# Kernel optimization log

Hardware: AMD Instinct MI355X
Metric: run time of the kernel (lower is better)

Reference implementation:

```python
import jax, jax.numpy as jnp
import numpy as np

B, L, H, E, K = 64, 200, 256, 8, 2
LN_EPS = 1e-5

def setup_inputs() -> dict:
    key = jax.random.key(0)
    ks = jax.random.split(key, 24)
    r = lambda k, *s: jax.random.normal(k, s, dtype=jnp.float32)
    w = lambda k, *s: 0.02 * jax.random.normal(k, s, dtype=jnp.float32)
    return {
        'text_emb': r(ks[0], B, L, H),
        'img_emb': r(ks[1], B, L, H),
        'item_emb': r(ks[2], B, L, H),
        'noise_t': r(ks[3], B, L, H),
        'noise_i': r(ks[4], B, L, H),
        'W_mu_t': w(ks[5], H, H), 'b_mu_t': jnp.zeros((H,), jnp.float32),
        'W_sg_t': w(ks[6], H, H), 'b_sg_t': jnp.zeros((H,), jnp.float32),
        'W_mu_i': w(ks[7], H, H), 'b_mu_i': jnp.zeros((H,), jnp.float32),
        'W_sg_i': w(ks[8], H, H), 'b_sg_i': jnp.zeros((H,), jnp.float32),
        'W_gate': w(ks[9], H, E), 'b_gate': jnp.zeros((E,), jnp.float32),
        'W_texp': w(ks[10], E, H, H), 'b_texp': jnp.zeros((E, H), jnp.float32),
        'W_iexp': w(ks[11], E, H, H), 'b_iexp': jnp.zeros((E, H), jnp.float32),
        'W_fuse': w(ks[12], 2 * H, H), 'b_fuse': jnp.zeros((H,), jnp.float32),
        'ln_g': jnp.ones((H,), jnp.float32), 'ln_b': jnp.zeros((H,), jnp.float32),
    }

def _topk_routing(z, W_gate, b_gate):
    # softmax over experts, keep top-k, renormalize (matches torch scatter_ version)
    weights = jax.nn.softmax(z @ W_gate + b_gate, axis=-1)   # [B,L,E]
    top_w, idx = jax.lax.top_k(weights, K)                   # [B,L,K]
    sparse = jnp.sum(jax.nn.one_hot(idx, E, dtype=weights.dtype) * top_w[..., None], axis=-2)
    return sparse / (jnp.sum(sparse, axis=-1, keepdims=True) + 1e-8)

def _layernorm(x, g, b):
    mu = jnp.mean(x, axis=-1, keepdims=True)
    var = jnp.mean(jnp.square(x - mu), axis=-1, keepdims=True)
    return (x - mu) * jax.lax.rsqrt(var + LN_EPS) * g + b

def reference(text_emb, img_emb, item_emb, noise_t, noise_i,
              W_mu_t, b_mu_t, W_sg_t, b_sg_t, W_mu_i, b_mu_i, W_sg_i, b_sg_i,
              W_gate, b_gate, W_texp, b_texp, W_iexp, b_iexp,
              W_fuse, b_fuse, ln_g, ln_b):
    # VAE-style reparameterization per modality
    t_mu = text_emb @ W_mu_t + b_mu_t
    t_sigma = jnp.exp(text_emb @ W_sg_t + b_sg_t)
    i_mu = img_emb @ W_mu_i + b_mu_i
    i_sigma = jnp.exp(img_emb @ W_sg_i + b_sg_i)
    t_z = t_mu + t_sigma * noise_t
    i_z = i_mu + i_sigma * noise_i
    # top-k gating
    t_gate = _topk_routing(t_z, W_gate, b_gate)   # [B,L,E]
    i_gate = _topk_routing(i_z, W_gate, b_gate)
    # dense all-expert stack + gated combine
    t_experts = jnp.einsum('blh,ehd->bled', t_z, W_texp) + b_texp  # [B,L,E,H]
    t_out = jnp.einsum('bled,ble->bld', t_experts, t_gate)
    i_experts = jnp.einsum('blh,ehd->bled', i_z, W_iexp) + b_iexp
    i_out = jnp.einsum('bled,ble->bld', i_experts, i_gate)
    # fusion: Linear(2H->H) -> LayerNorm -> ReLU, residual with item_emb
    cat = jnp.concatenate([t_out, i_out], axis=-1)
    fused = jax.nn.relu(_layernorm(cat @ W_fuse + b_fuse, ln_g, ln_b))
    fusion = item_emb + fused
    return fusion, t_mu, t_sigma, i_mu, i_sigma
```

## Files before the change

### kernel.cpp

```cpp
#include <hip/hip_runtime.h>
#include <hip/hip_bf16.h>
#include <math.h>

#define NTOK 12800
#define HD 256
#define SOUT (NTOK * HD)

typedef __attribute__((ext_vector_type(8))) short short8_t;
typedef __attribute__((ext_vector_type(4))) float f32x4;

__device__ __forceinline__ unsigned short f2b(float f) {
    union { float f; unsigned u; } v; v.f = f;
    unsigned r = (v.u + 0x7FFFu + ((v.u >> 16) & 1u)) >> 16;
    return (unsigned short)r;
}
__device__ __forceinline__ float b2f(unsigned short s) {
    union { unsigned u; float f; } v; v.u = ((unsigned)s) << 16;
    return v.f;
}
__device__ __forceinline__ void glds16(const void* g, void* l) {
    __builtin_amdgcn_global_load_lds(
        (const __attribute__((address_space(1))) void*)g,
        (__attribute__((address_space(3))) void*)l, 16, 0, 0);
}
__device__ __forceinline__ short8_t add_bf16x8(short8_t a, short8_t b) {
    union { unsigned short u[8]; short8_t v; } ua, ub, r;
    ua.v = a; ub.v = b;
#pragma unroll
    for (int i = 0; i < 8; ++i) r.u[i] = f2b(b2f(ua.u[i]) + b2f(ub.u[i]));
    return r.v;
}

__global__ __launch_bounds__(256) void prepW_kernel(
    const float* __restrict__ W_texp, const float* __restrict__ W_iexp,
    const float* __restrict__ W_mu_t, const float* __restrict__ W_sg_t,
    const float* __restrict__ W_mu_i, const float* __restrict__ W_sg_i,
    const float* __restrict__ W_fuse,
    unsigned short* __restrict__ wt_t, unsigned short* __restrict__ wt_i,
    unsigned short* __restrict__ wt_f,
    unsigned short* __restrict__ wpk_th, unsigned short* __restrict__ wpk_tl,
    unsigned short* __restrict__ wpk_ih, unsigned short* __restrict__ wpk_il)
{
    const int z = blockIdx.y;
    const float* src;
    unsigned short* dsth;
    unsigned short* dstl = nullptr;
    int dstride = 256, koff = 0, rowoff = 0;
    if (z < 8)       { src = W_texp + (size_t)z * 65536;       dsth = wt_t + (size_t)z * 65536; }
    else if (z < 16) { src = W_iexp + (size_t)(z - 8) * 65536; dsth = wt_i + (size_t)(z - 8) * 65536; }
    else if (z == 16){ src = W_mu_t; dsth = wpk_th; dstl = wpk_tl; }
    else if (z == 17){ src = W_sg_t; dsth = wpk_th; dstl = wpk_tl; rowoff = 256; }
    else if (z == 18){ src = W_mu_i; dsth = wpk_ih; dstl = wpk_il; }
    else if (z == 19){ src = W_sg_i; dsth = wpk_ih; dstl = wpk_il; rowoff = 256; }
    else if (z == 20){ src = W_fuse;         dsth = wt_f; dstride = 512; koff = 0;   }
    else             { src = W_fuse + 65536; dsth = wt_f; dstride = 512; koff = 256; }

    const int tk = (blockIdx.x >> 2) * 64;
    const int td = (blockIdx.x & 3) * 64;
    __shared__ float T[64][68];
    const int t = threadIdx.x;
    {
        const int r = t >> 2, c0 = (t & 3) * 16;
        const float* s = &src[(size_t)(tk + r) * 256 + td + c0];
#pragma unroll
        for (int j = 0; j < 4; ++j)
            *reinterpret_cast<float4*>(&T[r][c0 + j * 4]) =
                *reinterpret_cast<const float4*>(&s[j * 4]);
    }
    __syncthreads();
    {
        const int d = t & 63, kc = (t >> 6) * 16;
        union { unsigned short s[16]; short8_t v[2]; } uh, ul;
#pragma unroll
        for (int j = 0; j < 16; ++j) {
            const float x = T[kc + j][d];
            uh.s[j] = f2b(x);
            ul.s[j] = f2b(x - b2f(uh.s[j]));
        }
        unsigned short* p = &dsth[(size_t)(rowoff + td + d) * dstride + koff + tk + kc];
        *reinterpret_cast<short8_t*>(p) = uh.v[0];
        *reinterpret_cast<short8_t*>(p + 8) = uh.v[1];
        if (dstl) {
            unsigned short* q = &dstl[(size_t)(rowoff + td + d) * 256 + tk + kc];
            *reinterpret_cast<short8_t*>(q) = ul.v[0];
            *reinterpret_cast<short8_t*>(q + 8) = ul.v[1];
        }
    }
}

__global__ __launch_bounds__(256) void cvt_kernel(
    const float* __restrict__ text, const float* __restrict__ img,
    unsigned short* __restrict__ ah_t, unsigned short* __restrict__ al_t,
    unsigned short* __restrict__ ah_i, unsigned short* __restrict__ al_i)
{
    const int mod = blockIdx.y;
    const float* src = mod ? img : text;
    unsigned short* dh = mod ? ah_i : ah_t;
    unsigned short* dl = mod ? al_i : al_t;
    const size_t base = ((size_t)blockIdx.x * 256 + threadIdx.x) * 8;
    const float4 v0 = *reinterpret_cast<const float4*>(&src[base]);
    const float4 v1 = *reinterpret_cast<const float4*>(&src[base + 4]);
    const float x[8] = { v0.x, v0.y, v0.z, v0.w, v1.x, v1.y, v1.z, v1.w };
    union { unsigned short u[8]; short8_t v; } qh, ql;
#pragma unroll
    for (int c = 0; c < 8; ++c) {
        qh.u[c] = f2b(x[c]);
        ql.u[c] = f2b(x[c] - b2f(qh.u[c]));
    }
    *reinterpret_cast<short8_t*>(&dh[base]) = qh.v;
    *reinterpret_cast<short8_t*>(&dl[base]) = ql.v;
}

__global__ __launch_bounds__(256) void reparam_mfma_kernel(
    const unsigned short* __restrict__ ah_t, const unsigned short* __restrict__ al_t,
    const unsigned short* __restrict__ ah_i, const unsigned short* __restrict__ al_i,
    const unsigned short* __restrict__ wpk_th, const unsigned short* __restrict__ wpk_tl,
    const unsigned short* __restrict__ wpk_ih, const unsigned short* __restrict__ wpk_il,
    const float* __restrict__ b_mu_t, const float* __restrict__ b_sg_t,
    const float* __restrict__ b_mu_i, const float* __restrict__ b_sg_i,
    float* __restrict__ o_tmu, float* __restrict__ o_tsig,
    float* __restrict__ o_imu, float* __restrict__ o_isig)
{
    const int mod = blockIdx.z;
    const unsigned short* Ah = mod ? ah_i : ah_t;
    const unsigned short* Al = mod ? al_i : al_t;
    const unsigned short* Wh = mod ? wpk_ih : wpk_th;
    const unsigned short* Wl = mod ? wpk_il : wpk_tl;
    const float* bmu = mod ? b_mu_i : b_mu_t;
    const float* bsg = mod ? b_sg_i : b_sg_t;
    float* omu = mod ? o_imu : o_tmu;
    float* osg = mod ? o_isig : o_tsig;

    __shared__ __align__(16) unsigned short AhS[2][4][64][8];
    __shared__ __align__(16) unsigned short AlS[2][4][64][8];
    __shared__ __align__(16) unsigned short BhS[2][4][128][8];
    __shared__ __align__(16) unsigned short BlS[2][4][128][8];

    const int tid = threadIdx.x;
    const int lane = tid & 63;
    const int w = tid >> 6;
    const int wr = w >> 1, wc = w & 1;
    const int lg = lane >> 4;
    const int lr = lane & 15;
    const int m0 = blockIdx.x * 64;
    const int n0 = blockIdx.y * 128;

    const int ar = tid >> 2, akc = tid & 3;
    const int bn = tid >> 1, bk0 = (tid & 1) * 2;

    {
        *reinterpret_cast<short8_t*>(&AhS[0][akc][ar][0]) =
            *reinterpret_cast<const short8_t*>(&Ah[(size_t)(m0 + ar) * HD + akc * 8]);
        *reinterpret_cast<short8_t*>(&AlS[0][akc][ar][0]) =
            *reinterpret_cast<const short8_t*>(&Al[(size_t)(m0 + ar) * HD + akc * 8]);
#pragma unroll
        for (int j = 0; j < 2; ++j) {
            const int kc = bk0 + j;
            *reinterpret_cast<short8_t*>(&BhS[0][kc][bn][0]) =
                *reinterpret_cast<const short8_t*>(&Wh[(size_t)(n0 + bn) * HD + kc * 8]);
            *reinterpret_cast<short8_t*>(&BlS[0][kc][bn][0]) =
                *reinterpret_cast<const short8_t*>(&Wl[(size_t)(n0 + bn) * HD + kc * 8]);
        }
    }
    __syncthreads();

    f32x4 acc[2][4];
#pragma unroll
    for (int mi = 0; mi < 2; ++mi)
#pragma unroll
        for (int ni = 0; ni < 4; ++ni)
            acc[mi][ni] = (f32x4){0.f, 0.f, 0.f, 0.f};

    for (int ks = 0; ks < 8; ++ks) {
        const int cur = ks & 1;
        short8_t rah, ral, rbh[2], rbl[2];
        if (ks < 7) {
            const int k1 = (ks + 1) * 32;
            rah = *reinterpret_cast<const short8_t*>(&Ah[(size_t)(m0 + ar) * HD + k1 + akc * 8]);
            ral = *reinterpret_cast<const short8_t*>(&Al[(size_t)(m0 + ar) * HD + k1 + akc * 8]);
#pragma unroll
            for (int j = 0; j < 2; ++j) {
                const int kc = bk0 + j;
                rbh[j] = *reinterpret_cast<const short8_t*>(&Wh[(size_t)(n0 + bn) * HD + k1 + kc * 8]);
                rbl[j] = *reinterpret_cast<const short8_t*>(&Wl[(size_t)(n0 + bn) * HD + k1 + kc * 8]);
            }
        }
        short8_t ahf[2], alf[2], bhf[4], blf[4];
#pragma unroll
        for (int mi = 0; mi < 2; ++mi) {
            ahf[mi] = *reinterpret_cast<const short8_t*>(&AhS[cur][lg][wr * 32 + mi * 16 + lr][0]);
            alf[mi] = *reinterpret_cast<const short8_t*>(&AlS[cur][lg][wr * 32 + mi * 16 + lr][0]);
        }
#pragma unroll
        for (int ni = 0; ni < 4; ++ni) {
            bhf[ni] = *reinterpret_cast<const short8_t*>(&BhS[cur][lg][wc * 64 + ni * 16 + lr][0]);
            blf[ni] = *reinterpret_cast<const short8_t*>(&BlS[cur][lg][wc * 64 + ni * 16 + lr][0]);
        }
#pragma unroll
        for (int mi = 0; mi < 2; ++mi)
#pragma unroll
            for (int ni = 0; ni < 4; ++ni) {
                acc[mi][ni] = __builtin_amdgcn_mfma_f32_16x16x32_bf16(ahf[mi], bhf[ni], acc[mi][ni], 0, 0, 0);
                acc[mi][ni] = __builtin_amdgcn_mfma_f32_16x16x32_bf16(ahf[mi], blf[ni], acc[mi][ni], 0, 0, 0);
                acc[mi][ni] = __builtin_amdgcn_mfma_f32_16x16x32_bf16(alf[mi], bhf[ni], acc[mi][ni], 0, 0, 0);
            }
        if (ks < 7) {
            const int nxt = cur ^ 1;
            *reinterpret_cast<short8_t*>(&AhS[nxt][akc][ar][0]) = rah;
            *reinterpret_cast<short8_t*>(&AlS[nxt][akc][ar][0]) = ral;
#pragma unroll
            for (int j = 0; j < 2; ++j) {
                const int kc = bk0 + j;
                *reinterpret_cast<short8_t*>(&BhS[nxt][kc][bn][0]) = rbh[j];
                *reinterpret_cast<short8_t*>(&BlS[nxt][kc][bn][0]) = rbl[j];
            }
        }
        __syncthreads();
    }

    const bool is_sg = (n0 >= 256);
    float bv[4];
    int cc[4];
#pragma unroll
    for (int ni = 0; ni < 4; ++ni) {
        const int dpk = n0 + wc * 64 + ni * 16 + lr;
        cc[ni] = is_sg ? dpk - 256 : dpk;
        bv[ni] = is_sg ? bsg[cc[ni]] : bmu[cc[ni]];
    }
    float* outp = is_sg ? osg : omu;
#pragma unroll
    for (int mi = 0; mi < 2; ++mi)
#pragma unroll
        for (int r = 0; r < 4; ++r) {
            const int row = m0 + wr * 32 + mi * 16 + lg * 4 + r;
#pragma unroll
            for (int ni = 0; ni < 4; ++ni) {
                const float v = acc[mi][ni][r] + bv[ni];
                outp[(size_t)row * HD + cc[ni]] = is_sg ? expf(v) : v;
            }
        }
}

__global__ __launch_bounds__(256) void gate_kernel(
    const float* __restrict__ o_tmu, const float* __restrict__ o_tsig,
    const float* __restrict__ o_imu, const float* __restrict__ o_isig,
    const float* __restrict__ noise_t, const float* __restrict__ noise_i,
    const float* __restrict__ Wg, const float* __restrict__ bg,
    unsigned short* __restrict__ tzb, unsigned short* __restrict__ izb,
    unsigned* __restrict__ sel_e, float2* __restrict__ sel_w)
{
    const int mod = blockIdx.y;
    const float* mu    = mod ? o_imu  : o_tmu;
    const float* sig   = mod ? o_isig : o_tsig;
    const float* noise = mod ? noise_i : noise_t;
    unsigned short* zb = mod ? izb : tzb;

    const int lane = threadIdx.x & 63;
    const int n = blockIdx.x * 4 + (threadIdx.x >> 6);
    const size_t off = (size_t)n * HD + lane * 4;
    const float4 m4 = *reinterpret_cast<const float4*>(&mu[off]);
    const float4 s4 = *reinterpret_cast<const float4*>(&sig[off]);
    const float4 n4 = *reinterpret_cast<const float4*>(&noise[off]);
    const float zz[4] = { fmaf(s4.x, n4.x, m4.x), fmaf(s4.y, n4.y, m4.y),
                          fmaf(s4.z, n4.z, m4.z), fmaf(s4.w, n4.w, m4.w) };
    ushort4 zb4;
    zb4.x = f2b(zz[0]); zb4.y = f2b(zz[1]); zb4.z = f2b(zz[2]); zb4.w = f2b(zz[3]);
    *reinterpret_cast<ushort4*>(&zb[off]) = zb4;

    float lg[8];
#pragma unroll
    for (int e = 0; e < 8; ++e) lg[e] = 0.f;
#pragma unroll
    for (int i = 0; i < 4; ++i) {
        const float* wr = &Wg[(size_t)(lane * 4 + i) * 8];
        const float4 w0 = *reinterpret_cast<const float4*>(wr);
        const float4 w1 = *reinterpret_cast<const float4*>(wr + 4);
        lg[0] = fmaf(zz[i], w0.x, lg[0]); lg[1] = fmaf(zz[i], w0.y, lg[1]);
        lg[2] = fmaf(zz[i], w0.z, lg[2]); lg[3] = fmaf(zz[i], w0.w, lg[3]);
        lg[4] = fmaf(zz[i], w1.x, lg[4]); lg[5] = fmaf(zz[i], w1.y, lg[5]);
        lg[6] = fmaf(zz[i], w1.z, lg[6]); lg[7] = fmaf(zz[i], w1.w, lg[7]);
    }
#pragma unroll
    for (int off2 = 32; off2; off2 >>= 1)
#pragma unroll
        for (int e = 0; e < 8; ++e) lg[e] += __shfl_down(lg[e], off2);

    if (lane == 0) {
        float m = -1e30f;
#pragma unroll
        for (int e = 0; e < 8; ++e) { lg[e] += bg[e]; m = fmaxf(m, lg[e]); }
        float p[8], s = 0.f;
#pragma unroll
        for (int e = 0; e < 8; ++e) { p[e] = expf(lg[e] - m); s += p[e]; }
        const float inv_s = 1.f / s;
#pragma unroll
        for (int e = 0; e < 8; ++e) p[e] *= inv_s;
        int e1 = 0;
#pragma unroll
        for (int e = 1; e < 8; ++e) if (p[e] > p[e1]) e1 = e;
        int e2 = (e1 == 0) ? 1 : 0;
#pragma unroll
        for (int e = 0; e < 8; ++e) if (e != e1 && p[e] > p[e2]) e2 = e;
        const float denom = 1.f / (p[e1] + p[e2] + 1e-8f);
        sel_e[(size_t)mod * NTOK + n] = (unsigned)e1 | ((unsigned)e2 << 8);
        sel_w[(size_t)mod * NTOK + n] = make_float2(p[e1] * denom, p[e2] * denom);
    }
}

__global__ __launch_bounds__(1024) void compact_kernel(
    const unsigned* __restrict__ sel_e, const float2* __restrict__ sel_w,
    unsigned* __restrict__ idx_list, float* __restrict__ wgt_list,
    unsigned* __restrict__ cnt)
{
    const int seg = blockIdx.x;
    const int mod = seg >> 3;
    const unsigned e = (unsigned)(seg & 7);
    const int tid = threadIdx.x;
    const int wid = tid >> 6, lane = tid & 63;
    __shared__ unsigned wsum[16];

    unsigned off = 0;
    unsigned* dst_i = idx_list + (size_t)seg * NTOK;
    float* dst_w = wgt_list + (size_t)seg * NTOK;

    for (int chunk = 0; chunk < NTOK; chunk += 1024) {
        const int n = chunk + tid;
        const bool valid = (n < NTOK);
        unsigned se = 0;
        float2 wv = make_float2(0.f, 0.f);
        if (valid) {
            se = sel_e[(size_t)mod * NTOK + n];
            wv = sel_w[(size_t)mod * NTOK + n];
        }
#pragma unroll
        for (int slot = 0; slot < 2; ++slot) {
            const unsigned es = slot ? ((se >> 8) & 0xffu) : (se & 0xffu);
            const bool pred = valid && (es == e);
            const unsigned long long mask = __ballot(pred);
            if (lane == 0) wsum[wid] = (unsigned)__popcll(mask);
            __syncthreads();
            unsigned prefix = 0, total = 0;
#pragma unroll
            for (int wI = 0; wI < 16; ++wI) {
                const unsigned c = wsum[wI];
                if (wI < wid) prefix += c;
                total += c;
            }
            if (pred) {
                const unsigned long long lt = ((unsigned long long)1 << lane) - 1ull;
                const unsigned pos = off + prefix + (unsigned)__popcll(mask & lt);
                dst_i[pos] = (unsigned)(n * 2 + slot);
                dst_w[pos] = slot ? wv.y : wv.x;
            }
            off += total;
            __syncthreads();
        }
    }
    if (tid == 0) cnt[seg * 32] = off;
}

__global__ __launch_bounds__(256) void expert_sparse_kernel(
    const unsigned short* __restrict__ tzb, const unsigned short* __restrict__ izb,
    const unsigned short* __restrict__ wt_t, const unsigned short* __restrict__ wt_i,
    const float* __restrict__ bx_t, const float* __restrict__ bx_i,
    const unsigned* __restrict__ idx_list, const float* __restrict__ wgt_list,
    const unsigned* __restrict__ cnt,
    unsigned short* __restrict__ slot_t, unsigned short* __restrict__ slot_i)
{
    const int chunk = blockIdx.x;
    const int e  = blockIdx.y >> 1;
    const int nh = blockIdx.y & 1;
    const int mod = blockIdx.z;
    const int seg = mod * 8 + e;
    const unsigned cnt_e = cnt[seg * 32];
    if ((unsigned)(chunk * 128) >= cnt_e) return;

    const unsigned short* Zb = mod ? izb : tzb;
    const unsigned short* Wt = mod ? wt_i : wt_t;
    const float* bx = mod ? bx_i : bx_t;
    unsigned short* outp = mod ? slot_i : slot_t;
    const int n0 = nh * 128;
    const size_t sb = (size_t)seg * NTOK + (size_t)chunk * 128;

    __shared__ __align__(16) unsigned short Ab[2][512][8];
    __shared__ __align__(16) unsigned short Bb[2][512][8];
    __shared__ float gw[128];
    __shared__ unsigned il[128];

    const int tid = threadIdx.x;
    const int lane = tid & 63;
    const int w = tid >> 6;
    const int wr = w >> 1, wc = w & 1;
    const int lg = lane >> 4;
    const int lr = lane & 15;

    if (tid < 128) {
        const bool v = (unsigned)(chunk * 128 + tid) < cnt_e;
        il[tid] = v ? idx_list[sb + tid] : (unsigned)(2 * NTOK);
        gw[tid] = v ? wgt_list[sb + tid] : 0.f;
    }

    const int c0 = w * 64 + lane;
    const int row0 = c0 >> 2,         kc0 = c0 & 3;
    const int row1 = (c0 + 256) >> 2, kc1 = (c0 + 256) & 3;
    const unsigned i0 = ((unsigned)(chunk * 128 + row0) < cnt_e)
                        ? idx_list[sb + row0] : (unsigned)(2 * NTOK);
    const unsigned i1 = ((unsigned)(chunk * 128 + row1) < cnt_e)
                        ? idx_list[sb + row1] : (unsigned)(2 * NTOK);
    const size_t atok0 = (size_t)(i0 >> 1) * HD;
    const size_t atok1 = (size_t)(i1 >> 1) * HD;
    const unsigned short* We_ = Wt + (size_t)e * 65536 + (size_t)n0 * HD;

#define SSTAGE(buf, ks_)                                                       \
    {                                                                          \
        glds16(&Zb[atok0 + (ks_) * 32 + kc0 * 8], &Ab[buf][w * 64][0]);        \
        glds16(&Zb[atok1 + (ks_) * 32 + kc1 * 8], &Ab[buf][256 + w * 64][0]);  \
        glds16(&We_[(size_t)row0 * HD + (ks_) * 32 + kc0 * 8],                 \
               &Bb[buf][w * 64][0]);                                           \
        glds16(&We_[(size_t)row1 * HD + (ks_) * 32 + kc1 * 8],                 \
               &Bb[buf][256 + w * 64][0]);                                     \
    }

    SSTAGE(0, 0);
    __syncthreads();

    f32x4 acc[4][4];
#pragma unroll
    for (int mi = 0; mi < 4; ++mi)
#pragma unroll
        for (int ni = 0; ni < 4; ++ni)
            acc[mi][ni] = (f32x4){0.f, 0.f, 0.f, 0.f};

    for (int ks = 0; ks < 8; ++ks) {
        const int cur = ks & 1;
        if (ks < 7) SSTAGE(cur ^ 1, ks + 1);
        short8_t af[4], bf[4];
#pragma unroll
        for (int mi = 0; mi < 4; ++mi)
            af[mi] = *reinterpret_cast<const short8_t*>(
                &Ab[cur][(wr * 64 + mi * 16 + lr) * 4 + lg][0]);
#pragma unroll
        for (int ni = 0; ni < 4; ++ni)
            bf[ni] = *reinterpret_cast<const short8_t*>(
                &Bb[cur][(wc * 64 + ni * 16 + lr) * 4 + lg][0]);
#pragma unroll
        for (int mi = 0; mi < 4; ++mi)
#pragma unroll
            for (int ni = 0; ni < 4; ++ni)
                acc[mi][ni] = __builtin_amdgcn_mfma_f32_16x16x32_bf16(
                    af[mi], bf[ni], acc[mi][ni], 0, 0, 0);
        __syncthreads();
    }
#undef SSTAGE

    float bv[4];
#pragma unroll
    for (int ni = 0; ni < 4; ++ni)
        bv[ni] = bx[(size_t)e * HD + n0 + wc * 64 + ni * 16 + lr];
#pragma unroll
    for (int mi = 0; mi < 4; ++mi)
#pragma unroll
        for (int r = 0; r < 4; ++r) {
            const int row_local = wr * 64 + mi * 16 + lg * 4 + r;
            const float wv = gw[row_local];
            const size_t tb = (size_t)il[row_local] * HD;
#pragma unroll
            for (int ni = 0; ni < 4; ++ni)
                outp[tb + n0 + wc * 64 + ni * 16 + lr] =
                    f2b(wv * (acc[mi][ni][r] + bv[ni]));
        }
}

__global__ __launch_bounds__(256) void fusegemm_mfma_kernel(
    const unsigned short* __restrict__ slot_t, const unsigned short* __restrict__ slot_i,
    const unsigned short* __restrict__ wtf, const float* __restrict__ bfuse,
    float* __restrict__ fused)
{
    __shared__ __align__(16) unsigned short AS[2][8][64][8];
    __shared__ __align__(16) unsigned short BS[2][8][128][8];

    const int tid = threadIdx.x;
    const int lane = tid & 63;
    const int w = tid >> 6;
    const int wr = w >> 1, wc = w & 1;
    const int lg = lane >> 4;
    const int lr = lane & 15;
    const int m0 = blockIdx.x * 64;
    const int n0 = blockIdx.y * 128;

    const int ar = tid >> 2, akc0 = (tid & 3) * 2;
    const int bn = tid >> 1, bkc0 = (tid & 1) * 4;
    const size_t tb = (size_t)(m0 + ar) * 2 * HD;

    {
#pragma unroll
        for (int j = 0; j < 2; ++j) {
            const int kc = akc0 + j;
            const short8_t s0 = *reinterpret_cast<const short8_t*>(&slot_t[tb + kc * 8]);
            const short8_t s1 = *reinterpret_cast<const short8_t*>(&slot_t[tb + HD + kc * 8]);
            *reinterpret_cast<short8_t*>(&AS[0][kc][ar][0]) = add_bf16x8(s0, s1);
        }
#pragma unroll
        for (int j = 0; j < 4; ++j) {
            const int kc = bkc0 + j;
            *reinterpret_cast<short8_t*>(&BS[0][kc][bn][0]) =
                *reinterpret_cast<const short8_t*>(&wtf[(size_t)(n0 + bn) * 512 + kc * 8]);
        }
    }
    __syncthreads();

    f32x4 acc[2][4];
#pragma unroll
    for (int mi = 0; mi < 2; ++mi)
#pragma unroll
        for (int ni = 0; ni < 4; ++ni)
            acc[mi][ni] = (f32x4){0.f, 0.f, 0.f, 0.f};

    for (int ks = 0; ks < 8; ++ks) {
        const int cur = ks & 1;
        short8_t ra[2], rbv[4];
        if (ks < 7) {
            const int ks2 = ks + 1;
            const unsigned short* sp = (ks2 < 4) ? slot_t : slot_i;
            const int kloc = (ks2 & 3) * 64;
#pragma unroll
            for (int j = 0; j < 2; ++j) {
                const int kc = akc0 + j;
                const short8_t s0 = *reinterpret_cast<const short8_t*>(
                    &sp[tb + kloc + kc * 8]);
                const short8_t s1 = *reinterpret_cast<const short8_t*>(
                    &sp[tb + HD + kloc + kc * 8]);
                ra[j] = add_bf16x8(s0, s1);
            }
#pragma unroll
            for (int j = 0; j < 4; ++j) {
                const int kc = bkc0 + j;
                rbv[j] = *reinterpret_cast<const short8_t*>(
                    &wtf[(size_t)(n0 + bn) * 512 + ks2 * 64 + kc * 8]);
            }
        }
#pragma unroll
        for (int s = 0; s < 2; ++s) {
            short8_t af[2], bf[4];
#pragma unroll
            for (int mi = 0; mi < 2; ++mi)
                af[mi] = *reinterpret_cast<const short8_t*>(
                    &AS[cur][s * 4 + lg][wr * 32 + mi * 16 + lr][0]);
#pragma unroll
            for (int ni = 0; ni < 4; ++ni)
                bf[ni] = *reinterpret_cast<const short8_t*>(
                    &BS[cur][s * 4 + lg][wc * 64 + ni * 16 + lr][0]);
#pragma unroll
            for (int mi = 0; mi < 2; ++mi)
#pragma unroll
                for (int ni = 0; ni < 4; ++ni)
                    acc[mi][ni] = __builtin_amdgcn_mfma_f32_16x16x32_bf16(
                        af[mi], bf[ni], acc[mi][ni], 0, 0, 0);
        }
        if (ks < 7) {
            const int nxt = cur ^ 1;
#pragma unroll
            for (int j = 0; j < 2; ++j)
                *reinterpret_cast<short8_t*>(&AS[nxt][akc0 + j][ar][0]) = ra[j];
#pragma unroll
            for (int j = 0; j < 4; ++j)
                *reinterpret_cast<short8_t*>(&BS[nxt][bkc0 + j][bn][0]) = rbv[j];
        }
        __syncthreads();
    }

    float bv[4];
    int cc[4];
#pragma unroll
    for (int ni = 0; ni < 4; ++ni) {
        cc[ni] = n0 + wc * 64 + ni * 16 + lr;
        bv[ni] = bfuse[cc[ni]];
    }
#pragma unroll
    for (int mi = 0; mi < 2; ++mi)
#pragma unroll
        for (int r = 0; r < 4; ++r) {
            const int row = m0 + wr * 32 + mi * 16 + lg * 4 + r;
#pragma unroll
            for (int ni = 0; ni < 4; ++ni)
                fused[(size_t)row * HD + cc[ni]] = acc[mi][ni][r] + bv[ni];
        }
}

__global__ __launch_bounds__(256) void ln_relu_res_kernel(
    const float* __restrict__ fused, const float* __restrict__ g,
    const float* __restrict__ b, const float* __restrict__ item,
    float* __restrict__ fusion)
{
    const int lane = threadIdx.x & 63;
    const int n = blockIdx.x * 4 + (threadIdx.x >> 6);
    const size_t off = (size_t)n * HD + lane * 4;
    const float4 x = *reinterpret_cast<const float4*>(&fused[off]);
    float s = x.x + x.y + x.z + x.w;
    float ss = x.x * x.x + x.y * x.y + x.z * x.z + x.w * x.w;
#pragma unroll
    for (int o = 32; o; o >>= 1) { s += __shfl_xor(s, o); ss += __shfl_xor(ss, o); }
    const float mean = s * (1.f / 256.f);
    const float var = ss * (1.f / 256.f) - mean * mean;
    const float rstd = rsqrtf(var + 1e-5f);
    const float4 gg = *reinterpret_cast<const float4*>(&g[lane * 4]);
    const float4 bb = *reinterpret_cast<const float4*>(&b[lane * 4]);
    const float4 it = *reinterpret_cast<const float4*>(&item[off]);
    float4 o4;
    o4.x = fmaxf((x.x - mean) * rstd * gg.x + bb.x, 0.f) + it.x;
    o4.y = fmaxf((x.y - mean) * rstd * gg.y + bb.y, 0.f) + it.y;
    o4.z = fmaxf((x.z - mean) * rstd * gg.z + bb.z, 0.f) + it.z;
    o4.w = fmaxf((x.w - mean) * rstd * gg.w + bb.w, 0.f) + it.w;
    *reinterpret_cast<float4*>(&fusion[off]) = o4;
}

extern "C" void kernel_launch(void* const* d_in, const int* in_sizes, int n_in,
                              void* d_out, int out_size, void* d_ws, size_t ws_size,
                              hipStream_t stream)
{
    const float* text    = (const float*)d_in[0];
    const float* img     = (const float*)d_in[1];
    const float* item    = (const float*)d_in[2];
    const float* noise_t = (const float*)d_in[3];
    const float* noise_i = (const float*)d_in[4];
    const float* W_mu_t  = (const float*)d_in[5];
    const float* b_mu_t  = (const float*)d_in[6];
    const float* W_sg_t  = (const float*)d_in[7];
    const float* b_sg_t  = (const float*)d_in[8];
    const float* W_mu_i  = (const float*)d_in[9];
    const float* b_mu_i  = (const float*)d_in[10];
    const float* W_sg_i  = (const float*)d_in[11];
    const float* b_sg_i  = (const float*)d_in[12];
    const float* W_gate  = (const float*)d_in[13];
    const float* b_gate  = (const float*)d_in[14];
    const float* W_texp  = (const float*)d_in[15];
    const float* b_texp  = (const float*)d_in[16];
    const float* W_iexp  = (const float*)d_in[17];
    const float* b_iexp  = (const float*)d_in[18];
    const float* W_fuse  = (const float*)d_in[19];
    const float* b_fuse  = (const float*)d_in[20];
    const float* ln_g    = (const float*)d_in[21];
    const float* ln_b    = (const float*)d_in[22];

    float* out    = (float*)d_out;
    float* fusion = out;
    float* o_tmu  = out + (size_t)SOUT;
    float* o_tsig = out + (size_t)2 * SOUT;
    float* o_imu  = out + (size_t)3 * SOUT;
    float* o_isig = out + (size_t)4 * SOUT;

    const size_t SLOTPAD = (size_t)(2 * NTOK + 256) * HD;
    unsigned short* slot_t = (unsigned short*)d_ws;
    unsigned short* slot_i = slot_t + SLOTPAD;
    unsigned short* tzb    = slot_i + SLOTPAD;
    unsigned short* izb    = tzb + (size_t)SOUT;
    unsigned short* wt_t   = izb + (size_t)SOUT;
    unsigned short* wt_i   = wt_t + (size_t)8 * 65536;
    unsigned short* wt_f   = wt_i + (size_t)8 * 65536;
    unsigned short* wpk_th = wt_f + (size_t)131072;
    unsigned short* wpk_tl = wpk_th + (size_t)131072;
    unsigned short* wpk_ih = wpk_tl + (size_t)131072;
    unsigned short* wpk_il = wpk_ih + (size_t)131072;
    unsigned* idx_list = (unsigned*)(wpk_il + (size_t)131072);
    float*    wgt_list = (float*)(idx_list + (size_t)16 * NTOK);
    unsigned* cnt      = (unsigned*)(wgt_list + (size_t)16 * NTOK);
    unsigned* sel_e    = cnt + 512;
    float2*   sel_w    = (float2*)(sel_e + (size_t)2 * NTOK);

    unsigned short* ah_t = slot_t;
    unsigned short* al_t = slot_t + (size_t)SOUT;
    unsigned short* ah_i = slot_i;
    unsigned short* al_i = slot_i + (size_t)SOUT;
    float* fused = (float*)tzb;

    prepW_kernel<<<dim3(16, 22), 256, 0, stream>>>(
        W_texp, W_iexp, W_mu_t, W_sg_t, W_mu_i, W_sg_i, W_fuse,
        wt_t, wt_i, wt_f, wpk_th, wpk_tl, wpk_ih, wpk_il);

    cvt_kernel<<<dim3(SOUT / 2048, 2), 256, 0, stream>>>(
        text, img, ah_t, al_t, ah_i, al_i);

    reparam_mfma_kernel<<<dim3(NTOK / 64, 4, 2), 256, 0, stream>>>(
        ah_t, al_t, ah_i, al_i, wpk_th, wpk_tl, wpk_ih, wpk_il,
        b_mu_t, b_sg_t, b_mu_i, b_sg_i,
        o_tmu, o_tsig, o_imu, o_isig);

    gate_kernel<<<dim3(NTOK / 4, 2), 256, 0, stream>>>(
        o_tmu, o_tsig, o_imu, o_isig, noise_t, noise_i,
        W_gate, b_gate, tzb, izb, sel_e, sel_w);

    compact_kernel<<<16, 1024, 0, stream>>>(
        sel_e, sel_w, idx_list, wgt_list, cnt);

    expert_sparse_kernel<<<dim3(100, 16, 2), 256, 0, stream>>>(
        tzb, izb, wt_t, wt_i, b_texp, b_iexp,
        idx_list, wgt_list, cnt, slot_t, slot_i);

    fusegemm_mfma_kernel<<<dim3(NTOK / 64, 2), 256, 0, stream>>>(
        slot_t, slot_i, wt_f, b_fuse, fused);

    ln_relu_res_kernel<<<NTOK / 4, 256, 0, stream>>>(fused, ln_g, ln_b, item, fusion);
}
```

Baseline: 148.3 us.

## Fuse reparameterization, z computation and partial gate logits into mu/sigma GEMM

Each GEMM block now computes matching 64-column tiles of both mu and sigma, so it can form z = mu + sigma*noise in its epilogue, write the bf16 z, and compute partial gate logits over its 64 columns into a small partials buffer. The separate gate kernel is removed, and the compaction kernel becomes a route kernel that sums the four partials and does softmax/top-2 itself. This avoids re-reading mu, sigma and noise from global memory and saves one launch, at the cost of more LDS per block (48 KB) and more accumulator registers.

New measurement: 159.0 us. 7.2% more time.

```diff
diff --git a/kernel.cpp b/kernel.cpp
--- a/kernel.cpp
+++ b/kernel.cpp
@@ -118,23 +118,36 @@
     const unsigned short* __restrict__ wpk_ih, const unsigned short* __restrict__ wpk_il,
     const float* __restrict__ b_mu_t, const float* __restrict__ b_sg_t,
     const float* __restrict__ b_mu_i, const float* __restrict__ b_sg_i,
+    const float* __restrict__ noise_t, const float* __restrict__ noise_i,
+    const float* __restrict__ Wg,
     float* __restrict__ o_tmu, float* __restrict__ o_tsig,
-    float* __restrict__ o_imu, float* __restrict__ o_isig)
+    float* __restrict__ o_imu, float* __restrict__ o_isig,
+    unsigned short* __restrict__ tzb, unsigned short* __restrict__ izb,
+    float* __restrict__ part)
 {
     const int mod = blockIdx.z;
+    const int dt = blockIdx.y;
+    const int d0 = dt * 64;
+    const int m0 = blockIdx.x * 64;
     const unsigned short* Ah = mod ? ah_i : ah_t;
     const unsigned short* Al = mod ? al_i : al_t;
     const unsigned short* Wh = mod ? wpk_ih : wpk_th;
     const unsigned short* Wl = mod ? wpk_il : wpk_tl;
-    const float* bmu = mod ? b_mu_i : b_mu_t;
-    const float* bsg = mod ? b_sg_i : b_sg_t;
+    const float* bmu   = mod ? b_mu_i : b_mu_t;
+    const float* bsg   = mod ? b_sg_i : b_sg_t;
+    const float* noise = mod ? noise_i : noise_t;
     float* omu = mod ? o_imu : o_tmu;
     float* osg = mod ? o_isig : o_tsig;
-
-    __shared__ __align__(16) unsigned short AhS[2][4][64][8];
-    __shared__ __align__(16) unsigned short AlS[2][4][64][8];
-    __shared__ __align__(16) unsigned short BhS[2][4][128][8];
-    __shared__ __align__(16) unsigned short BlS[2][4][128][8];
+    unsigned short* zb = mod ? izb : tzb;
+
+    __shared__ __align__(16) unsigned char smem[49152];
+    typedef unsigned short (*Stage)[4][64][8];
+    Stage AhS = (Stage)(smem);
+    Stage AlS = (Stage)(smem + 8192);
+    Stage BMh = (Stage)(smem + 16384);
+    Stage BMl = (Stage)(smem + 24576);
+    Stage BSh = (Stage)(smem + 32768);
+    Stage BSl = (Stage)(smem + 40960);
 
     const int tid = threadIdx.x;
     const int lane = tid & 63;
@@ -142,173 +155,135 @@
     const int wr = w >> 1, wc = w & 1;
     const int lg = lane >> 4;
     const int lr = lane & 15;
-    const int m0 = blockIdx.x * 64;
-    const int n0 = blockIdx.y * 128;
 
     const int ar = tid >> 2, akc = tid & 3;
-    const int bn = tid >> 1, bk0 = (tid & 1) * 2;
+    const int bn = tid >> 2, bkc = tid & 3;
 
     {
         *reinterpret_cast<short8_t*>(&AhS[0][akc][ar][0]) =
             *reinterpret_cast<const short8_t*>(&Ah[(size_t)(m0 + ar) * HD + akc * 8]);
         *reinterpret_cast<short8_t*>(&AlS[0][akc][ar][0]) =
             *reinterpret_cast<const short8_t*>(&Al[(size_t)(m0 + ar) * HD + akc * 8]);
-#pragma unroll
-        for (int j = 0; j < 2; ++j) {
-            const int kc = bk0 + j;
-            *reinterpret_cast<short8_t*>(&BhS[0][kc][bn][0]) =
-                *reinterpret_cast<const short8_t*>(&Wh[(size_t)(n0 + bn) * HD + kc * 8]);
-            *reinterpret_cast<short8_t*>(&BlS[0][kc][bn][0]) =
-                *reinterpret_cast<const short8_t*>(&Wl[(size_t)(n0 + bn) * HD + kc * 8]);
-        }
+        *reinterpret_cast<short8_t*>(&BMh[0][bkc][bn][0]) =
+            *reinterpret_cast<const short8_t*>(&Wh[(size_t)(d0 + bn) * HD + bkc * 8]);
+        *reinterpret_cast<short8_t*>(&BMl[0][bkc][bn][0]) =
+            *reinterpret_cast<const short8_t*>(&Wl[(size_t)(d0 + bn) * HD + bkc * 8]);
+        *reinterpret_cast<short8_t*>(&BSh[0][bkc][bn][0]) =
+            *reinterpret_cast<const short8_t*>(&Wh[(size_t)(256 + d0 + bn) * HD + bkc * 8]);
+        *reinterpret_cast<short8_t*>(&BSl[0][bkc][bn][0]) =
+            *reinterpret_cast<const short8_t*>(&Wl[(size_t)(256 + d0 + bn) * HD + bkc * 8]);
     }
     __syncthreads();
 
-    f32x4 acc[2][4];
+    f32x4 accM[2][2], accS[2][2];
 #pragma unroll
     for (int mi = 0; mi < 2; ++mi)
 #pragma unroll
-        for (int ni = 0; ni < 4; ++ni)
-            acc[mi][ni] = (f32x4){0.f, 0.f, 0.f, 0.f};
+        for (int ni = 0; ni < 2; ++ni) {
+            accM[mi][ni] = (f32x4){0.f, 0.f, 0.f, 0.f};
+            accS[mi][ni] = (f32x4){0.f, 0.f, 0.f, 0.f};
+        }
 
     for (int ks = 0; ks < 8; ++ks) {
         const int cur = ks & 1;
-        short8_t rah, ral, rbh[2], rbl[2];
+        short8_t rah, ral, rmh, rml, rsh, rsl;
         if (ks < 7) {
             const int k1 = (ks + 1) * 32;
             rah = *reinterpret_cast<const short8_t*>(&Ah[(size_t)(m0 + ar) * HD + k1 + akc * 8]);
             ral = *reinterpret_cast<const short8_t*>(&Al[(size_t)(m0 + ar) * HD + k1 + akc * 8]);
-#pragma unroll
-            for (int j = 0; j < 2; ++j) {
-                const int kc = bk0 + j;
-                rbh[j] = *reinterpret_cast<const short8_t*>(&Wh[(size_t)(n0 + bn) * HD + k1 + kc * 8]);
-                rbl[j] = *reinterpret_cast<const short8_t*>(&Wl[(size_t)(n0 + bn) * HD + k1 + kc * 8]);
-            }
-        }
-        short8_t ahf[2], alf[2], bhf[4], blf[4];
+            rmh = *reinterpret_cast<const short8_t*>(&Wh[(size_t)(d0 + bn) * HD + k1 + bkc * 8]);
+            rml = *reinterpret_cast<const short8_t*>(&Wl[(size_t)(d0 + bn) * HD + k1 + bkc * 8]);
+            rsh = *reinterpret_cast<const short8_t*>(&Wh[(size_t)(256 + d0 + bn) * HD + k1 + bkc * 8]);
+            rsl = *reinterpret_cast<const short8_t*>(&Wl[(size_t)(256 + d0 + bn) * HD + k1 + bkc * 8]);
+        }
+        short8_t ahf[2], alf[2], bmh[2], bml[2], bsh[2], bsl[2];
 #pragma unroll
         for (int mi = 0; mi < 2; ++mi) {
             ahf[mi] = *reinterpret_cast<const short8_t*>(&AhS[cur][lg][wr * 32 + mi * 16 + lr][0]);
             alf[mi] = *reinterpret_cast<const short8_t*>(&AlS[cur][lg][wr * 32 + mi * 16 + lr][0]);
         }
 #pragma unroll
-        for (int ni = 0; ni < 4; ++ni) {
-            bhf[ni] = *reinterpret_cast<const short8_t*>(&BhS[cur][lg][wc * 64 + ni * 16 + lr][0]);
-            blf[ni] = *reinterpret_cast<const short8_t*>(&BlS[cur][lg][wc * 64 + ni * 16 + lr][0]);
+        for (int ni = 0; ni < 2; ++ni) {
+            bmh[ni] = *reinterpret_cast<const short8_t*>(&BMh[cur][lg][wc * 32 + ni * 16 + lr][0]);
+            bml[ni] = *reinterpret_cast<const short8_t*>(&BMl[cur][lg][wc * 32 + ni * 16 + lr][0]);
+            bsh[ni] = *reinterpret_cast<const short8_t*>(&BSh[cur][lg][wc * 32 + ni * 16 + lr][0]);
+            bsl[ni] = *reinterpret_cast<const short8_t*>(&BSl[cur][lg][wc * 32 + ni * 16 + lr][0]);
         }
 #pragma unroll
         for (int mi = 0; mi < 2; ++mi)
 #pragma unroll
-            for (int ni = 0; ni < 4; ++ni) {
-                acc[mi][ni] = __builtin_amdgcn_mfma_f32_16x16x32_bf16(ahf[mi], bhf[ni], acc[mi][ni], 0, 0, 0);
-                acc[mi][ni] = __builtin_amdgcn_mfma_f32_16x16x32_bf16(ahf[mi], blf[ni], acc[mi][ni], 0, 0, 0);
-                acc[mi][ni] = __builtin_amdgcn_mfma_f32_16x16x32_bf16(alf[mi], bhf[ni], acc[mi][ni], 0, 0, 0);
+            for (int ni = 0; ni < 2; ++ni) {
+                accM[mi][ni] = __builtin_amdgcn_mfma_f32_16x16x32_bf16(ahf[mi], bmh[ni], accM[mi][ni], 0, 0, 0);
+                accM[mi][ni] = __builtin_amdgcn_mfma_f32_16x16x32_bf16(ahf[mi], bml[ni], accM[mi][ni], 0, 0, 0);
+                accM[mi][ni] = __builtin_amdgcn_mfma_f32_16x16x32_bf16(alf[mi], bmh[ni], accM[mi][ni], 0, 0, 0);
+                accS[mi][ni] = __builtin_amdgcn_mfma_f32_16x16x32_bf16(ahf[mi], bsh[ni], accS[mi][ni], 0, 0, 0);
+                accS[mi][ni] = __builtin_amdgcn_mfma_f32_16x16x32_bf16(ahf[mi], bsl[ni], accS[mi][ni], 0, 0, 0);
+                accS[mi][ni] = __builtin_amdgcn_mfma_f32_16x16x32_bf16(alf[mi], bsh[ni], accS[mi][ni], 0, 0, 0);
             }
         if (ks < 7) {
             const int nxt = cur ^ 1;
             *reinterpret_cast<short8_t*>(&AhS[nxt][akc][ar][0]) = rah;
             *reinterpret_cast<short8_t*>(&AlS[nxt][akc][ar][0]) = ral;
-#pragma unroll
-            for (int j = 0; j < 2; ++j) {
-                const int kc = bk0 + j;
-                *reinterpret_cast<short8_t*>(&BhS[nxt][kc][bn][0]) = rbh[j];
-                *reinterpret_cast<short8_t*>(&BlS[nxt][kc][bn][0]) = rbl[j];
+            *reinterpret_cast<short8_t*>(&BMh[nxt][bkc][bn][0]) = rmh;
+            *reinterpret_cast<short8_t*>(&BMl[nxt][bkc][bn][0]) = rml;
+            *reinterpret_cast<short8_t*>(&BSh[nxt][bkc][bn][0]) = rsh;
+            *reinterpret_cast<short8_t*>(&BSl[nxt][bkc][bn][0]) = rsl;
+        }
+        __syncthreads();
+    }
+
+    float (*zs)[68] = (float (*)[68])(smem);
+    float* wgs = (float*)(smem + 17920);
+
+    int cc[2];
+    float bmv[2], bsv[2];
+#pragma unroll
+    for (int ni = 0; ni < 2; ++ni) {
+        cc[ni] = d0 + wc * 32 + ni * 16 + lr;
+        bmv[ni] = bmu[cc[ni]];
+        bsv[ni] = bsg[cc[ni]];
+    }
+#pragma unroll
+    for (int mi = 0; mi < 2; ++mi)
+#pragma unroll
+        for (int r = 0; r < 4; ++r) {
+            const int rl = wr * 32 + mi * 16 + lg * 4 + r;
+            const int row = m0 + rl;
+#pragma unroll
+            for (int ni = 0; ni < 2; ++ni) {
+                const size_t off = (size_t)row * HD + cc[ni];
+                const float mu = accM[mi][ni][r] + bmv[ni];
+                const float sg = expf(accS[mi][ni][r] + bsv[ni]);
+                const float z = fmaf(sg, noise[off], mu);
+                omu[off] = mu;
+                osg[off] = sg;
+                zb[off] = f2b(z);
+                zs[rl][wc * 32 + ni * 16 + lr] = z;
             }
         }
-        __syncthreads();
-    }
-
-    const bool is_sg = (n0 >= 256);
-    float bv[4];
-    int cc[4];
-#pragma unroll
-    for (int ni = 0; ni < 4; ++ni) {
-        const int dpk = n0 + wc * 64 + ni * 16 + lr;
-        cc[ni] = is_sg ? dpk - 256 : dpk;
-        bv[ni] = is_sg ? bsg[cc[ni]] : bmu[cc[ni]];
-    }
-    float* outp = is_sg ? osg : omu;
-#pragma unroll
-    for (int mi = 0; mi < 2; ++mi)
-#pragma unroll
-        for (int r = 0; r < 4; ++r) {
-            const int row = m0 + wr * 32 + mi * 16 + lg * 4 + r;
-#pragma unroll
-            for (int ni = 0; ni < 4; ++ni) {
-                const float v = acc[mi][ni][r] + bv[ni];
-                outp[(size_t)row * HD + cc[ni]] = is_sg ? expf(v) : v;
-            }
-        }
-}
-
-__global__ __launch_bounds__(256) void gate_kernel(
-    const float* __restrict__ o_tmu, const float* __restrict__ o_tsig,
-    const float* __restrict__ o_imu, const float* __restrict__ o_isig,
-    const float* __restrict__ noise_t, const float* __restrict__ noise_i,
-    const float* __restrict__ Wg, const float* __restrict__ bg,
-    unsigned short* __restrict__ tzb, unsigned short* __restrict__ izb,
-    unsigned* __restrict__ sel_e, float2* __restrict__ sel_w)
-{
-    const int mod = blockIdx.y;
-    const float* mu    = mod ? o_imu  : o_tmu;
-    const float* sig   = mod ? o_isig : o_tsig;
-    const float* noise = mod ? noise_i : noise_t;
-    unsigned short* zb = mod ? izb : tzb;
-
-    const int lane = threadIdx.x & 63;
-    const int n = blockIdx.x * 4 + (threadIdx.x >> 6);
-    const size_t off = (size_t)n * HD + lane * 4;
-    const float4 m4 = *reinterpret_cast<const float4*>(&mu[off]);
-    const float4 s4 = *reinterpret_cast<const float4*>(&sig[off]);
-    const float4 n4 = *reinterpret_cast<const float4*>(&noise[off]);
-    const float zz[4] = { fmaf(s4.x, n4.x, m4.x), fmaf(s4.y, n4.y, m4.y),
-                          fmaf(s4.z, n4.z, m4.z), fmaf(s4.w, n4.w, m4.w) };
-    ushort4 zb4;
-    zb4.x = f2b(zz[0]); zb4.y = f2b(zz[1]); zb4.z = f2b(zz[2]); zb4.w = f2b(zz[3]);
-    *reinterpret_cast<ushort4*>(&zb[off]) = zb4;
-
-    float lg[8];
-#pragma unroll
-    for (int e = 0; e < 8; ++e) lg[e] = 0.f;
-#pragma unroll
-    for (int i = 0; i < 4; ++i) {
-        const float* wr = &Wg[(size_t)(lane * 4 + i) * 8];
-        const float4 w0 = *reinterpret_cast<const float4*>(wr);
-        const float4 w1 = *reinterpret_cast<const float4*>(wr + 4);
-        lg[0] = fmaf(zz[i], w0.x, lg[0]); lg[1] = fmaf(zz[i], w0.y, lg[1]);
-        lg[2] = fmaf(zz[i], w0.z, lg[2]); lg[3] = fmaf(zz[i], w0.w, lg[3]);
-        lg[4] = fmaf(zz[i], w1.x, lg[4]); lg[5] = fmaf(zz[i], w1.y, lg[5]);
-        lg[6] = fmaf(zz[i], w1.z, lg[6]); lg[7] = fmaf(zz[i], w1.w, lg[7]);
-    }
-#pragma unroll
-    for (int off2 = 32; off2; off2 >>= 1)
-#pragma unroll
-        for (int e = 0; e < 8; ++e) lg[e] += __shfl_down(lg[e], off2);
-
-    if (lane == 0) {
-        float m = -1e30f;
-#pragma unroll
-        for (int e = 0; e < 8; ++e) { lg[e] += bg[e]; m = fmaxf(m, lg[e]); }
-        float p[8], s = 0.f;
-#pragma unroll
-        for (int e = 0; e < 8; ++e) { p[e] = expf(lg[e] - m); s += p[e]; }
-        const float inv_s = 1.f / s;
-#pragma unroll
-        for (int e = 0; e < 8; ++e) p[e] *= inv_s;
-        int e1 = 0;
-#pragma unroll
-        for (int e = 1; e < 8; ++e) if (p[e] > p[e1]) e1 = e;
-        int e2 = (e1 == 0) ? 1 : 0;
-#pragma unroll
-        for (int e = 0; e < 8; ++e) if (e != e1 && p[e] > p[e2]) e2 = e;
-        const float denom = 1.f / (p[e1] + p[e2] + 1e-8f);
-        sel_e[(size_t)mod * NTOK + n] = (unsigned)e1 | ((unsigned)e2 << 8);
-        sel_w[(size_t)mod * NTOK + n] = make_float2(p[e1] * denom, p[e2] * denom);
-    }
-}
-
-__global__ __launch_bounds__(1024) void compact_kernel(
-    const unsigned* __restrict__ sel_e, const float2* __restrict__ sel_w,
+    if (tid < 128)
+        reinterpret_cast<float4*>(wgs)[tid] =
+            reinterpret_cast<const float4*>(&Wg[(size_t)d0 * 8])[tid];
+    __syncthreads();
+
+    {
+        const int rl = tid >> 2;
+        const int e0 = (tid & 3) * 2;
+        float l0 = 0.f, l1 = 0.f;
+#pragma unroll
+        for (int d = 0; d < 64; ++d) {
+            const float zv = zs[rl][d];
+            l0 = fmaf(zv, wgs[d * 8 + e0], l0);
+            l1 = fmaf(zv, wgs[d * 8 + e0 + 1], l1);
+        }
+        float* pp = part + (((size_t)(mod * 4 + dt) * NTOK) + (m0 + rl)) * 8;
+        pp[e0] = l0;
+        pp[e0 + 1] = l1;
+    }
+}
+
+__global__ __launch_bounds__(1024) void route_kernel(
+    const float* __restrict__ part, const float* __restrict__ bg,
     unsigned* __restrict__ idx_list, float* __restrict__ wgt_list,
     unsigned* __restrict__ cnt)
 {
@@ -326,16 +301,42 @@
     for (int chunk = 0; chunk < NTOK; chunk += 1024) {
         const int n = chunk + tid;
         const bool valid = (n < NTOK);
-        unsigned se = 0;
-        float2 wv = make_float2(0.f, 0.f);
+        int e1 = 0, e2 = 1;
+        float w1 = 0.f, w2 = 0.f;
         if (valid) {
-            se = sel_e[(size_t)mod * NTOK + n];
-            wv = sel_w[(size_t)mod * NTOK + n];
+            float lg[8];
+#pragma unroll
+            for (int k = 0; k < 8; ++k) lg[k] = bg[k];
+#pragma unroll
+            for (int dt = 0; dt < 4; ++dt) {
+                const float* pp = part + (((size_t)(mod * 4 + dt) * NTOK) + n) * 8;
+                const float4 p0 = *reinterpret_cast<const float4*>(pp);
+                const float4 p1 = *reinterpret_cast<const float4*>(pp + 4);
+                lg[0] += p0.x; lg[1] += p0.y; lg[2] += p0.z; lg[3] += p0.w;
+                lg[4] += p1.x; lg[5] += p1.y; lg[6] += p1.z; lg[7] += p1.w;
+            }
+            float m = -1e30f;
+#pragma unroll
+            for (int k = 0; k < 8; ++k) m = fmaxf(m, lg[k]);
+            float p[8], s = 0.f;
+#pragma unroll
+            for (int k = 0; k < 8; ++k) { p[k] = expf(lg[k] - m); s += p[k]; }
+            const float inv_s = 1.f / s;
+#pragma unroll
+            for (int k = 0; k < 8; ++k) p[k] *= inv_s;
+            e1 = 0;
+#pragma unroll
+            for (int k = 1; k < 8; ++k) if (p[k] > p[e1]) e1 = k;
+            e2 = (e1 == 0) ? 1 : 0;
+#pragma unroll
+            for (int k = 0; k < 8; ++k) if (k != e1 && p[k] > p[e2]) e2 = k;
+            const float denom = 1.f / (p[e1] + p[e2] + 1e-8f);
+            w1 = p[e1] * denom;
+            w2 = p[e2] * denom;
         }
 #pragma unroll
         for (int slot = 0; slot < 2; ++slot) {
-            const unsigned es = slot ? ((se >> 8) & 0xffu) : (se & 0xffu);
-            const bool pred = valid && (es == e);
+            const bool pred = valid && ((unsigned)(slot ? e2 : e1) == e);
             const unsigned long long mask = __ballot(pred);
             if (lane == 0) wsum[wid] = (unsigned)__popcll(mask);
             __syncthreads();
@@ -350,7 +351,7 @@
                 const unsigned long long lt = ((unsigned long long)1 << lane) - 1ull;
                 const unsigned pos = off + prefix + (unsigned)__popcll(mask & lt);
                 dst_i[pos] = (unsigned)(n * 2 + slot);
-                dst_w[pos] = slot ? wv.y : wv.x;
+                dst_w[pos] = slot ? w2 : w1;
             }
             off += total;
             __syncthreads();
@@ -664,8 +665,7 @@
     unsigned* idx_list = (unsigned*)(wpk_il + (size_t)131072);
     float*    wgt_list = (float*)(idx_list + (size_t)16 * NTOK);
     unsigned* cnt      = (unsigned*)(wgt_list + (size_t)16 * NTOK);
-    unsigned* sel_e    = cnt + 512;
-    float2*   sel_w    = (float2*)(sel_e + (size_t)2 * NTOK);
+    float*    part     = (float*)(cnt + 512);
 
     unsigned short* ah_t = slot_t;
     unsigned short* al_t = slot_t + (size_t)SOUT;
@@ -682,15 +682,11 @@
 
     reparam_mfma_kernel<<<dim3(NTOK / 64, 4, 2), 256, 0, stream>>>(
         ah_t, al_t, ah_i, al_i, wpk_th, wpk_tl, wpk_ih, wpk_il,
-        b_mu_t, b_sg_t, b_mu_i, b_sg_i,
-        o_tmu, o_tsig, o_imu, o_isig);
-
-    gate_kernel<<<dim3(NTOK / 4, 2), 256, 0, stream>>>(
-        o_tmu, o_tsig, o_imu, o_isig, noise_t, noise_i,
-        W_gate, b_gate, tzb, izb, sel_e, sel_w);
-
-    compact_kernel<<<16, 1024, 0, stream>>>(
-        sel_e, sel_w, idx_list, wgt_list, cnt);
+        b_mu_t, b_sg_t, b_mu_i, b_sg_i, noise_t, noise_i, W_gate,
+        o_tmu, o_tsig, o_imu, o_isig, tzb, izb, part);
+
+    route_kernel<<<16, 1024, 0, stream>>>(
+        part, b_gate, idx_list, wgt_list, cnt);
 
     expert_sparse_kernel<<<dim3(100, 16, 2), 256, 0, stream>>>(
         tzb, izb, wt_t, wt_i, b_texp, b_iexp,
```
